# Performance work log

Measured on AMD Instinct MI355X. Metric: run time of the kernel, lower is better.

The kernel has to match this reference:

```python
import jax, jax.numpy as jnp
import numpy as np

B, S, D, O, R, E = 2, 4096, 4096, 4096, 256, 8
SCALE = 2.0

def setup_inputs() -> dict:
    key = jax.random.key(0)
    k_x, k_t, k_w, k_a, k_b = jax.random.split(key, 5)
    x = jax.random.normal(k_x, (B, S, D), dtype=jnp.float32)
    token_type = jax.random.randint(k_t, (S,), 0, E, dtype=jnp.int64)
    # weight_base: [out_features, in_features] as required by F.linear
    weight_base = jax.random.normal(k_w, (O, D), dtype=jnp.float32) * 0.02
    # LoRA stacks: lora_A [E, D, R], lora_B [E, R, O]. (Original inits B to zeros;
    # we use small random values so the LoRA path is numerically non-trivial.)
    lora_A = jax.random.normal(k_a, (E, D, R), dtype=jnp.float32) * 0.02
    lora_B = jax.random.normal(k_b, (E, R, O), dtype=jnp.float32) * 0.02
    return {"x": x, "weight_base": weight_base, "lora_A": lora_A,
            "lora_B": lora_B, "token_type": token_type}

def reference(x, weight_base, lora_A, lora_B, token_type):
    # base GEMM: F.linear(x, W) = x @ W.T  -> [B, S, O]
    base = jnp.einsum('bsd,od->bso', x, weight_base)
    # per-expert low-rank projection: h[e,b,s,:] = x[b,s,:] @ lora_A[e]
    h = jnp.einsum('bsd,edr->ebsr', x, lora_A)              # [E, B, S, R]
    # dispatch: zero out tokens not routed to expert e (token_type partitions S)
    onehot = jax.nn.one_hot(token_type, E, dtype=x.dtype)   # [S, E]
    h = h * onehot.T[:, None, :, None]                      # mask over (e, s)
    # combine: sum over experts of masked h @ lora_B[e]
    lora = jnp.einsum('ebsr,ero->bso', h, lora_B)           # [B, S, O]
    # every token has token_type in [0, E), so scatter covers all positions:
    # result = base + scale * expert_lora everywhere
    return base + SCALE * lora
```

## Files before the change

### kernel.cpp

```cpp
#include <hip/hip_runtime.h>

#define S_TOK 4096
#define D_DIM 4096
#define O_DIM 4096
#define R_DIM 256
#define E_EXP 8
#define NTOK  8192
#define KSPLIT 4

typedef __bf16 bf16x8 __attribute__((ext_vector_type(8)));
typedef float  f32x4  __attribute__((ext_vector_type(4)));

__device__ __forceinline__ unsigned short f2bf(float f) {
  unsigned int u = __float_as_uint(f);
  u += 0x7FFFu + ((u >> 16) & 1u);
  return (unsigned short)(u >> 16);
}
__device__ __forceinline__ float bf2f(unsigned short h) {
  return __uint_as_float(((unsigned int)h) << 16);
}

__device__ __forceinline__ void gload_lds16(const unsigned short* g, unsigned short* l) {
  __builtin_amdgcn_global_load_lds((const __attribute__((address_space(1))) void*)g,
                                   (__attribute__((address_space(3))) void*)l, 16, 0, 0);
}

#define PIPE_FENCE(N)                                                        \
  do {                                                                       \
    asm volatile("s_waitcnt vmcnt(" #N ")\n\ts_barrier" ::: "memory");       \
    __builtin_amdgcn_sched_barrier(0);                                       \
  } while (0)

__global__ void prologue(const float* __restrict__ x, const float* __restrict__ wb,
                         const float* __restrict__ la, const float* __restrict__ lb,
                         unsigned short* __restrict__ X16, unsigned short* __restrict__ W16,
                         unsigned short* __restrict__ A16t, unsigned short* __restrict__ B16t,
                         const int* __restrict__ tt, int* __restrict__ token_perm,
                         int* __restrict__ inv_perm, int* __restrict__ tile_e,
                         int* __restrict__ tile_j0, int* __restrict__ tile_jend,
                         int* __restrict__ ntiles_out) {
  __shared__ int sm[10256];
  const int b = blockIdx.x, t = threadIdx.x;
  if (b >= 40960) {
    int* ltt   = sm;
    int* lc    = sm + 4096;
    int* ssl   = sm + 6144;
    int* basee = sm + 10240;
    int* cnte  = sm + 10248;
    for (int s = t; s < S_TOK; s += 256) ltt[s] = tt[s];
    __syncthreads();
    int c[8] = {0,0,0,0,0,0,0,0};
    #pragma unroll
    for (int i = 0; i < 16; i++) { int e = ltt[t * 16 + i]; c[e]++; }
    #pragma unroll
    for (int e = 0; e < 8; e++) lc[t * 8 + e] = c[e];
    __syncthreads();
    if (t < 8) {
      int run = 0;
      for (int qq = 0; qq < 256; qq++) { int tmp = lc[qq * 8 + t]; lc[qq * 8 + t] = run; run += tmp; }
      cnte[t] = run;
    }
    __syncthreads();
    if (t == 0) { int tot = 0; for (int e = 0; e < 8; e++) { basee[e] = tot; tot += cnte[e]; } }
    __syncthreads();
    int off[8];
    #pragma unroll
    for (int e = 0; e < 8; e++) off[e] = basee[e] + lc[t * 8 + e];
    #pragma unroll
    for (int i = 0; i < 16; i++) { int s = t * 16 + i; int e = ltt[s]; ssl[off[e]++] = s; }
    __syncthreads();
    for (int j = t; j < NTOK; j += 256) {
      int row = ((j & 1) << 12) + ssl[j >> 1];
      token_perm[j] = row;
      inv_perm[row] = j;
    }
    if (t == 0) {
      int nt = 0;
      for (int e = 0; e < 8; e++) {
        int js = 2 * basee[e], je = js + 2 * cnte[e];
        for (int j0 = js; j0 < je; j0 += 128) {
          tile_e[nt] = e; tile_j0[nt] = j0;
          tile_jend[nt] = (je < j0 + 128) ? je : (j0 + 128);
          nt++;
        }
      }
      *ntiles_out = nt;
    }
    return;
  }
  if (b < 24576) {
    const float* in  = (b < 16384) ? x : wb;
    unsigned short* out = (b < 16384) ? X16 : W16;
    size_t g = (size_t)((b < 16384) ? b : (b - 16384)) * 256 + t;
    const float4* i4 = (const float4*)in;
    float4 a = i4[g * 2], c = i4[g * 2 + 1];
    union { unsigned short h[8]; int4 v; } u;
    u.h[0] = f2bf(a.x); u.h[1] = f2bf(a.y); u.h[2] = f2bf(a.z); u.h[3] = f2bf(a.w);
    u.h[4] = f2bf(c.x); u.h[5] = f2bf(c.y); u.h[6] = f2bf(c.z); u.h[7] = f2bf(c.w);
    ((int4*)out)[g] = u.v;
    return;
  }
  unsigned short (*tile)[33] = (unsigned short (*)[33])sm;
  const float* in; unsigned short* out; int P, Q, pt, qt, e;
  if (b < 32768) {
    int b2 = b - 24576; e = b2 >> 10; int rem = b2 & 1023;
    in = la; out = A16t; P = D_DIM; Q = R_DIM;
    pt = (rem >> 3) * 32; qt = (rem & 7) * 32;
  } else {
    int b3 = b - 32768; e = b3 >> 10; int rem = b3 & 1023;
    in = lb; out = B16t; P = R_DIM; Q = D_DIM;
    pt = (rem & 7) * 32; qt = (rem >> 3) * 32;
  }
  const float* ie = in + (size_t)e * P * Q;
  unsigned short* oe = out + (size_t)e * P * Q;
  int tx = t & 31, ty = t >> 5;
  #pragma unroll
  for (int i = 0; i < 32; i += 8) {
    int p = pt + ty + i, q = qt + tx;
    tile[ty + i][tx] = f2bf(ie[(size_t)p * Q + q]);
  }
  __syncthreads();
  #pragma unroll
  for (int i = 0; i < 32; i += 8) {
    int q = qt + ty + i, p = pt + tx;
    oe[(size_t)q * P + p] = tile[tx][ty + i];
  }
}

template<int FUSED>
__global__ __launch_bounds__(512, 2) void gemm256_dense(
    const unsigned short* __restrict__ A, const unsigned short* __restrict__ B,
    float* __restrict__ C, const unsigned short* __restrict__ lout,
    const int* __restrict__ invp) {
  __shared__ __align__(16) unsigned short ldsA[2][2][8192];
  __shared__ __align__(16) unsigned short ldsB[2][2][8192];
  int b = blockIdx.x;
  int xc = b & 7, q = b >> 3;
  const int bm = (xc >> 1) * 8 + (q >> 3);
  const int bn = (xc & 1) * 8 + (q & 7);
  const int tid = threadIdx.x, l = tid & 63, w = tid >> 6;
  const int wm = w >> 2, wn = w & 3;

  const unsigned short *srcA0, *srcA1, *srcB0, *srcB1;
  {
    int i0 = tid, r0 = i0 >> 2;
    int c0 = ((i0 & 3) * 16) ^ (((r0 >> 1) & 3) << 4);
    srcA0 = A + (size_t)(bm * 256 + r0) * 4096 + (c0 >> 1);
    srcB0 = B + (size_t)(bn * 256 + r0) * 4096 + (c0 >> 1);
    int i1 = 512 + tid, r1 = i1 >> 2;
    int c1 = ((i1 & 3) * 16) ^ (((r1 >> 1) & 3) << 4);
    srcA1 = A + (size_t)(bm * 256 + r1) * 4096 + (c1 >> 1);
    srcB1 = B + (size_t)(bn * 256 + r1) * 4096 + (c1 >> 1);
  }
  const int d0 = tid * 8;

  const int lane15 = l & 15, kb16 = (l >> 4) * 16;
  int offA[8], offB[4];
  #pragma unroll
  for (int m = 0; m < 8; m++) {
    int r = wm * 128 + m * 16 + lane15;
    offA[m] = r * 64 + (kb16 ^ (((r >> 1) & 3) << 4));
  }
  #pragma unroll
  for (int n = 0; n < 4; n++) {
    int r = wn * 64 + n * 16 + lane15;
    offB[n] = r * 64 + (kb16 ^ (((r >> 1) & 3) << 4));
  }

  f32x4 acc[8][4];
  #pragma unroll
  for (int m = 0; m < 8; m++)
    #pragma unroll
    for (int n = 0; n < 4; n++) acc[m][n] = (f32x4){0.f, 0.f, 0.f, 0.f};

  bf16x8 Ab0[4], Ab1[4], Bb0[4], Bb1[4];

#define STAGE_A(tt, kh) do { int _o = (tt) * 64 + (kh) * 32;                  \
    gload_lds16(srcA0 + _o, &ldsA[(tt) & 1][kh][d0]);                         \
    gload_lds16(srcA1 + _o, &ldsA[(tt) & 1][kh][d0 + 4096]); } while (0)
#define STAGE_B(tt, kh) do { int _o = (tt) * 64 + (kh) * 32;                  \
    gload_lds16(srcB0 + _o, &ldsB[(tt) & 1][kh][d0]);                         \
    gload_lds16(srcB1 + _o, &ldsB[(tt) & 1][kh][d0 + 4096]); } while (0)
#define RD_A(RING, QQ, KS, BUF) do {                                          \
    const char* _s = (const char*)&ldsA[RING][KS][0];                         \
    BUF[0] = *(const bf16x8*)(_s + offA[(QQ) * 4 + 0]);                       \
    BUF[1] = *(const bf16x8*)(_s + offA[(QQ) * 4 + 1]);                       \
    BUF[2] = *(const bf16x8*)(_s + offA[(QQ) * 4 + 2]);                       \
    BUF[3] = *(const bf16x8*)(_s + offA[(QQ) * 4 + 3]); } while (0)
#define RD_B(RING, KS, BUF) do {                                              \
    const char* _s = (const char*)&ldsB[RING][KS][0];                         \
    BUF[0] = *(const bf16x8*)(_s + offB[0]);                                  \
    BUF[1] = *(const bf16x8*)(_s + offB[1]);                                  \
    BUF[2] = *(const bf16x8*)(_s + offB[2]);                                  \
    BUF[3] = *(const bf16x8*)(_s + offB[3]); } while (0)
#define PRIO_MFMA(Q, AB, BB) do {                                             \
    __builtin_amdgcn_s_setprio(1);                                            \
    _Pragma("unroll")                                                         \
    for (int mm = 0; mm < 4; mm++)                                            \
      _Pragma("unroll")                                                       \
      for (int nn = 0; nn < 4; nn++)                                          \
        acc[(Q) * 4 + mm][nn] = __builtin_amdgcn_mfma_f32_16x16x32_bf16(      \
            AB[mm], BB[nn], acc[(Q) * 4 + mm][nn], 0, 0, 0);                  \
    __builtin_amdgcn_s_setprio(0); } while (0)

  STAGE_A(0, 0); STAGE_B(0, 0); STAGE_A(0, 1); STAGE_B(0, 1);
  STAGE_A(1, 0); STAGE_B(1, 0);
  PIPE_FENCE(4);
  RD_B(0, 0, Bb0); RD_A(0, 0, 0, Ab0);

  #pragma unroll 1
  for (int t = 0; t < 62; ++t) {
    const int r = t & 1, nr = r ^ 1;
    RD_A(r, 1, 0, Ab1); STAGE_A(t + 1, 1);
    PRIO_MFMA(0, Ab0, Bb0);
    RD_B(r, 1, Bb1); RD_A(r, 0, 1, Ab0); STAGE_B(t + 1, 1);
    PRIO_MFMA(1, Ab1, Bb0);
    PIPE_FENCE(4);
    RD_A(r, 1, 1, Ab1); STAGE_A(t + 2, 0);
    PRIO_MFMA(0, Ab0, Bb1);
    RD_B(nr, 0, Bb0); RD_A(nr, 0, 0, Ab0); STAGE_B(t + 2, 0);
    PRIO_MFMA(1, Ab1, Bb1);
    PIPE_FENCE(4);
  }
  RD_A(0, 1, 0, Ab1); STAGE_A(63, 1); PRIO_MFMA(0, Ab0, Bb0);
  RD_B(0, 1, Bb1); RD_A(0, 0, 1, Ab0); STAGE_B(63, 1); PRIO_MFMA(1, Ab1, Bb0);
  PIPE_FENCE(4);
  RD_A(0, 1, 1, Ab1); PRIO_MFMA(0, Ab0, Bb1);
  RD_B(1, 0, Bb0); RD_A(1, 0, 0, Ab0); PRIO_MFMA(1, Ab1, Bb1);
  PIPE_FENCE(0);
  RD_A(1, 1, 0, Ab1); PRIO_MFMA(0, Ab0, Bb0);
  RD_B(1, 1, Bb1); RD_A(1, 0, 1, Ab0); PRIO_MFMA(1, Ab1, Bb0);
  RD_A(1, 1, 1, Ab1); PRIO_MFMA(0, Ab0, Bb1);
  PRIO_MFMA(1, Ab1, Bb1);

#undef STAGE_A
#undef STAGE_B
#undef RD_A
#undef RD_B
#undef PRIO_MFMA

  const int rowbase = bm * 256 + wm * 128;
  const int colbase = bn * 256 + wn * 64;
  #pragma unroll
  for (int m = 0; m < 8; m++)
    #pragma unroll
    for (int v = 0; v < 4; v++) {
      int rrow = rowbase + m * 16 + (l >> 4) * 4 + v;
      float lv0 = 0.f, lv1 = 0.f, lv2 = 0.f, lv3 = 0.f;
      if (FUSED) {
        int jr = invp[rrow];
        const unsigned short* lr = lout + (size_t)jr * O_DIM + colbase + lane15;
        lv0 = bf2f(lr[0]); lv1 = bf2f(lr[16]); lv2 = bf2f(lr[32]); lv3 = bf2f(lr[48]);
      }
      size_t base = (size_t)rrow * O_DIM + colbase + lane15;
      C[base]      = acc[m][0][v] + lv0;
      C[base + 16] = acc[m][1][v] + lv1;
      C[base + 32] = acc[m][2][v] + lv2;
      C[base + 48] = acc[m][3][v] + lv3;
    }
}

template<int MODE>
__global__ __launch_bounds__(256, 2) void gemm_nt(
    const unsigned short* __restrict__ Aop, const unsigned short* __restrict__ Bop,
    unsigned short* __restrict__ outU,
    const int* __restrict__ perm, const int* __restrict__ tile_e,
    const int* __restrict__ tile_j0, const int* __restrict__ tile_jend,
    const int* __restrict__ ntiles, int K) {
  int bm = blockIdx.x, bn = blockIdx.y;
  if (bm >= *ntiles) return;
  int e = tile_e[bm], j0 = tile_j0[bm], jend = tile_jend[bm];
  const int kc = (MODE == 1) ? blockIdx.z : 0;
  const int t = threadIdx.x, l = t & 63, w = t >> 6;
  const int wm = w >> 1, wn = w & 1;
  __shared__ __align__(16) unsigned short ldsA[4][4096];
  __shared__ __align__(16) unsigned short ldsB[4][4096];

  const unsigned short *sA0, *sA1, *sB0, *sB1;
  {
    int i0 = t, r0 = i0 >> 2;
    int c0 = ((i0 & 3) * 16) ^ (((r0 >> 1) & 3) << 4);
    int i1 = 256 + t, r1 = i1 >> 2;
    int c1 = ((i1 & 3) * 16) ^ (((r1 >> 1) & 3) << 4);
    int ja = j0 + r0; if (ja > jend - 1) ja = jend - 1;
    int jb = j0 + r1; if (jb > jend - 1) jb = jend - 1;
    int g0 = (MODE == 1) ? perm[ja] : ja;
    int g1 = (MODE == 1) ? perm[jb] : jb;
    sA0 = Aop + (size_t)g0 * K + kc * 1024 + (c0 >> 1);
    sA1 = Aop + (size_t)g1 * K + kc * 1024 + (c1 >> 1);
    const unsigned short* bp = Bop + ((MODE == 1) ? (size_t)e * R_DIM * D_DIM
                                                  : (size_t)e * O_DIM * R_DIM);
    sB0 = bp + (size_t)(bn * 128 + r0) * K + kc * 1024 + (c0 >> 1);
    sB1 = bp + (size_t)(bn * 128 + r1) * K + kc * 1024 + (c1 >> 1);
  }
  const int d0 = t * 8;

  const int lane15 = l & 15, kb16 = (l >> 4) * 16;
  int offA[4], offB[4];
  #pragma unroll
  for (int m = 0; m < 4; m++) {
    int r = wm * 64 + m * 16 + lane15;
    offA[m] = r * 64 + (kb16 ^ (((r >> 1) & 3) << 4));
  }
  #pragma unroll
  for (int n = 0; n < 4; n++) {
    int r = wn * 64 + n * 16 + lane15;
    offB[n] = r * 64 + (kb16 ^ (((r >> 1) & 3) << 4));
  }

  f32x4 acc[4][4];
  #pragma unroll
  for (int m = 0; m < 4; m++)
    #pragma unroll
    for (int n = 0; n < 4; n++) acc[m][n] = (f32x4){0.f, 0.f, 0.f, 0.f};

  auto stage = [&](int tt) {
    const int ring = tt & 3;
    const int go = tt * 32;
    gload_lds16(sA0 + go, &ldsA[ring][d0]);
    gload_lds16(sA1 + go, &ldsA[ring][d0 + 2048]);
    gload_lds16(sB0 + go, &ldsB[ring][d0]);
    gload_lds16(sB1 + go, &ldsB[ring][d0 + 2048]);
  };

  auto body = [&](int ring) {
    const char* bA = (const char*)&ldsA[ring][0];
    const char* bB = (const char*)&ldsB[ring][0];
    bf16x8 a[4], bb[4];
    #pragma unroll
    for (int m = 0; m < 4; m++) a[m] = *(const bf16x8*)(bA + offA[m]);
    #pragma unroll
    for (int n = 0; n < 4; n++) bb[n] = *(const bf16x8*)(bB + offB[n]);
    __builtin_amdgcn_s_setprio(1);
    #pragma unroll
    for (int m = 0; m < 4; m++)
      #pragma unroll
      for (int n = 0; n < 4; n++)
        acc[m][n] = __builtin_amdgcn_mfma_f32_16x16x32_bf16(a[m], bb[n], acc[m][n], 0, 0, 0);
    __builtin_amdgcn_s_setprio(0);
  };

  const int nk = (MODE == 1) ? 32 : (K / 32);
  stage(0); stage(1); stage(2);
  PIPE_FENCE(8);
  #pragma unroll 1
  for (int kt = 0; kt < nk - 3; ++kt) {
    stage(kt + 3);
    body(kt & 3);
    PIPE_FENCE(8);
  }
  body((nk - 3) & 3);
  PIPE_FENCE(4);
  body((nk - 2) & 3);
  PIPE_FENCE(0);
  body((nk - 1) & 3);

  const int rowbase = j0 + wm * 64;
  const int colbase = bn * 128 + wn * 64;
  #pragma unroll
  for (int m = 0; m < 4; m++) {
    #pragma unroll
    for (int n = 0; n < 4; n++) {
      #pragma unroll
      for (int v = 0; v < 4; v++) {
        int r = rowbase + m * 16 + (l >> 4) * 4 + v;
        int cc = colbase + n * 16 + lane15;
        if (r < jend) {
          if (MODE == 1) {
            outU[(size_t)kc * (NTOK * R_DIM) + (size_t)r * R_DIM + cc] = f2bf(acc[m][n][v]);
          } else {
            outU[(size_t)r * O_DIM + cc] = f2bf(2.0f * acc[m][n][v]);
          }
        }
      }
    }
  }
}

__global__ void reduce_h(const unsigned short* __restrict__ hp, unsigned short* __restrict__ h16) {
  size_t g = (size_t)blockIdx.x * 256 + threadIdx.x;
  float s[8] = {0,0,0,0,0,0,0,0};
  #pragma unroll
  for (int c = 0; c < KSPLIT; c++) {
    int4 v = ((const int4*)hp)[g + (size_t)c * (NTOK * R_DIM / 8)];
    const unsigned short* us = (const unsigned short*)&v;
    #pragma unroll
    for (int i = 0; i < 8; i++) s[i] += bf2f(us[i]);
  }
  union { unsigned short h[8]; int4 v; } u;
  #pragma unroll
  for (int i = 0; i < 8; i++) u.h[i] = f2bf(s[i]);
  ((int4*)h16)[g] = u.v;
}

#define X16_OFF   ((size_t)0)
#define W16_OFF   ((size_t)67108864)
#define A16T_OFF  ((size_t)100663296)
#define B16T_OFF  ((size_t)117440512)
#define H16S_OFF  ((size_t)134217728)
#define PERM_OFF  ((size_t)138412032)
#define INVP_OFF  ((size_t)138444800)
#define TILEE_OFF ((size_t)138477568)
#define TILEJ0_OFF ((size_t)138478080)
#define TILEJE_OFF ((size_t)138478592)
#define NT_OFF    ((size_t)138479104)
#define HP16_OFF  ((size_t)138479616)
#define LOUT_OFF  ((size_t)155256832)

extern "C" void kernel_launch(void* const* d_in, const int* in_sizes, int n_in,
                              void* d_out, int out_size, void* d_ws, size_t ws_size,
                              hipStream_t stream) {
  const float* x  = (const float*)d_in[0];
  const float* wb = (const float*)d_in[1];
  const float* la = (const float*)d_in[2];
  const float* lb = (const float*)d_in[3];
  const int* tok  = (const int*)d_in[4];
  float* out = (float*)d_out;

  char* ws = (char*)d_ws;
  unsigned short* X16  = (unsigned short*)(ws + X16_OFF);
  unsigned short* W16  = (unsigned short*)(ws + W16_OFF);
  unsigned short* A16t = (unsigned short*)(ws + A16T_OFF);
  unsigned short* B16t = (unsigned short*)(ws + B16T_OFF);
  unsigned short* H16s = (unsigned short*)(ws + H16S_OFF);
  unsigned short* HP16 = (unsigned short*)(ws + HP16_OFF);
  unsigned short* LOUT = (unsigned short*)(ws + LOUT_OFF);
  int* perm  = (int*)(ws + PERM_OFF);
  int* invp  = (int*)(ws + INVP_OFF);
  int* tl_e  = (int*)(ws + TILEE_OFF);
  int* tl_j0 = (int*)(ws + TILEJ0_OFF);
  int* tl_je = (int*)(ws + TILEJE_OFF);
  int* nt    = (int*)(ws + NT_OFF);

  prologue<<<40961, 256, 0, stream>>>(x, wb, la, lb, X16, W16, A16t, B16t,
                                      tok, perm, invp, tl_e, tl_j0, tl_je, nt);

  gemm_nt<1><<<dim3(71, 2, KSPLIT), 256, 0, stream>>>(X16, A16t, HP16,
                                                      perm, tl_e, tl_j0, tl_je, nt, D_DIM);
  reduce_h<<<1024, 256, 0, stream>>>(HP16, H16s);
  gemm_nt<3><<<dim3(71, 32), 256, 0, stream>>>(H16s, B16t, LOUT,
                                               perm, tl_e, tl_j0, tl_je, nt, R_DIM);
  gemm256_dense<1><<<512, 512, 0, stream>>>(X16, W16, out, LOUT, invp);
}
```

Baseline: 458.7 us.

## Restructure dense GEMM main loop into four quadrant phases with new LDS layout

The base dense GEMM now stages each LDS buffer by output quadrant (64-row A halves and 32-row B halves, full 64-wide K per row) instead of by K-half. Each of the four phases per K-tile reads its A/B fragments, issues one quadrant's global-to-LDS load, barriers, then runs 16 MFMAs on that quadrant. The XOR swizzle changes to a row-based 8-way pattern to avoid LDS bank conflicts. The aim is finer-grained interleaving of loads and MFMAs. The cost is extra s_barrier instructions per tile and different vmcnt fence depths.

```diff
diff --git a/kernel.cpp b/kernel.cpp
--- a/kernel.cpp
+++ b/kernel.cpp
@@ -28,6 +28,11 @@
 #define PIPE_FENCE(N)                                                        \
   do {                                                                       \
     asm volatile("s_waitcnt vmcnt(" #N ")\n\ts_barrier" ::: "memory");       \
+    __builtin_amdgcn_sched_barrier(0);                                       \
+  } while (0)
+#define BARX                                                                 \
+  do {                                                                       \
+    asm volatile("s_barrier" ::: "memory");                                  \
     __builtin_amdgcn_sched_barrier(0);                                       \
   } while (0)
 
@@ -128,7 +133,7 @@
 }
 
 template<int FUSED>
-__global__ __launch_bounds__(512, 2) void gemm256_dense(
+__global__ __launch_bounds__(512, 2) void gemm256_q(
     const unsigned short* __restrict__ A, const unsigned short* __restrict__ B,
     float* __restrict__ C, const unsigned short* __restrict__ lout,
     const int* __restrict__ invp) {
@@ -141,30 +146,27 @@
   const int tid = threadIdx.x, l = tid & 63, w = tid >> 6;
   const int wm = w >> 2, wn = w & 3;
 
-  const unsigned short *srcA0, *srcA1, *srcB0, *srcB1;
-  {
-    int i0 = tid, r0 = i0 >> 2;
-    int c0 = ((i0 & 3) * 16) ^ (((r0 >> 1) & 3) << 4);
-    srcA0 = A + (size_t)(bm * 256 + r0) * 4096 + (c0 >> 1);
-    srcB0 = B + (size_t)(bn * 256 + r0) * 4096 + (c0 >> 1);
-    int i1 = 512 + tid, r1 = i1 >> 2;
-    int c1 = ((i1 & 3) * 16) ^ (((r1 >> 1) & 3) << 4);
-    srcA1 = A + (size_t)(bm * 256 + r1) * 4096 + (c1 >> 1);
-    srcB1 = B + (size_t)(bn * 256 + r1) * 4096 + (c1 >> 1);
-  }
-  const int d0 = tid * 8;
-
-  const int lane15 = l & 15, kb16 = (l >> 4) * 16;
-  int offA[8], offB[4];
-  #pragma unroll
-  for (int m = 0; m < 8; m++) {
-    int r = wm * 128 + m * 16 + lane15;
-    offA[m] = r * 64 + (kb16 ^ (((r >> 1) & 3) << 4));
-  }
-  #pragma unroll
-  for (int n = 0; n < 4; n++) {
-    int r = wn * 64 + n * 16 + lane15;
-    offB[n] = r * 64 + (kb16 ^ (((r >> 1) & 3) << 4));
+  const int u0 = tid >> 3, j0s = tid & 7;
+  const int ksw = ((j0s ^ (u0 & 7)) * 8);
+  const unsigned short* srcA0 = A + (size_t)(bm * 256 + u0) * 4096 + ksw;
+  const unsigned short* srcA1 = A + (size_t)(bm * 256 + 128 + u0) * 4096 + ksw;
+  const int brB0 = ((u0 >> 5) << 6) + (u0 & 31);
+  const int brB1 = (((64 + u0) >> 5) << 6) + (u0 & 31);
+  const unsigned short* srcB0 = B + (size_t)(bn * 256 + brB0) * 4096 + ksw;
+  const unsigned short* srcB1 = B + (size_t)(bn * 256 + brB1) * 4096 + ksw;
+
+  const int lane15 = l & 15, kbase = (l >> 4) * 16;
+  const int lsw = (lane15 & 7) << 4;
+  int offA[4], offB[2];
+  #pragma unroll
+  for (int j = 0; j < 4; j++) {
+    int u = wm * 64 + j * 16 + lane15;
+    offA[j] = u * 128 + (kbase ^ lsw);
+  }
+  #pragma unroll
+  for (int i = 0; i < 2; i++) {
+    int u = wn * 32 + i * 16 + lane15;
+    offB[i] = u * 128 + (kbase ^ lsw);
   }
 
   f32x4 acc[8][4];
@@ -173,71 +175,74 @@
     #pragma unroll
     for (int n = 0; n < 4; n++) acc[m][n] = (f32x4){0.f, 0.f, 0.f, 0.f};
 
-  bf16x8 Ab0[4], Ab1[4], Bb0[4], Bb1[4];
-
-#define STAGE_A(tt, kh) do { int _o = (tt) * 64 + (kh) * 32;                  \
-    gload_lds16(srcA0 + _o, &ldsA[(tt) & 1][kh][d0]);                         \
-    gload_lds16(srcA1 + _o, &ldsA[(tt) & 1][kh][d0 + 4096]); } while (0)
-#define STAGE_B(tt, kh) do { int _o = (tt) * 64 + (kh) * 32;                  \
-    gload_lds16(srcB0 + _o, &ldsB[(tt) & 1][kh][d0]);                         \
-    gload_lds16(srcB1 + _o, &ldsB[(tt) & 1][kh][d0 + 4096]); } while (0)
-#define RD_A(RING, QQ, KS, BUF) do {                                          \
-    const char* _s = (const char*)&ldsA[RING][KS][0];                         \
-    BUF[0] = *(const bf16x8*)(_s + offA[(QQ) * 4 + 0]);                       \
-    BUF[1] = *(const bf16x8*)(_s + offA[(QQ) * 4 + 1]);                       \
-    BUF[2] = *(const bf16x8*)(_s + offA[(QQ) * 4 + 2]);                       \
-    BUF[3] = *(const bf16x8*)(_s + offA[(QQ) * 4 + 3]); } while (0)
-#define RD_B(RING, KS, BUF) do {                                              \
-    const char* _s = (const char*)&ldsB[RING][KS][0];                         \
-    BUF[0] = *(const bf16x8*)(_s + offB[0]);                                  \
-    BUF[1] = *(const bf16x8*)(_s + offB[1]);                                  \
-    BUF[2] = *(const bf16x8*)(_s + offB[2]);                                  \
-    BUF[3] = *(const bf16x8*)(_s + offB[3]); } while (0)
-#define PRIO_MFMA(Q, AB, BB) do {                                             \
+#define STAGE_A(TT, H) do {                                                   \
+    gload_lds16(srcA0 + (size_t)(H) * 262144 + (TT) * 64,                     \
+                &ldsA[(TT) & 1][H][tid * 8]);                                 \
+    gload_lds16(srcA1 + (size_t)(H) * 262144 + (TT) * 64,                     \
+                &ldsA[(TT) & 1][H][4096 + tid * 8]); } while (0)
+#define STAGE_B(TT, H) do {                                                   \
+    gload_lds16(srcB0 + (size_t)(H) * 131072 + (TT) * 64,                     \
+                &ldsB[(TT) & 1][H][tid * 8]);                                 \
+    gload_lds16(srcB1 + (size_t)(H) * 131072 + (TT) * 64,                     \
+                &ldsB[(TT) & 1][H][4096 + tid * 8]); } while (0)
+#define NOSTAGE do {} while (0)
+
+#define PH(RING, QM, QN, STAGE_STMT, TRAILER) do {                            \
+    const char* _a = (const char*)&ldsA[RING][QM][0];                         \
+    const char* _b = (const char*)&ldsB[RING][QN][0];                         \
+    bf16x8 a0_[4], a1_[4], b0_[2], b1_[2];                                    \
+    _Pragma("unroll")                                                         \
+    for (int j = 0; j < 4; j++) {                                             \
+      a0_[j] = *(const bf16x8*)(_a + offA[j]);                                \
+      a1_[j] = *(const bf16x8*)(_a + (offA[j] ^ 64));                         \
+    }                                                                         \
+    _Pragma("unroll")                                                         \
+    for (int i = 0; i < 2; i++) {                                             \
+      b0_[i] = *(const bf16x8*)(_b + offB[i]);                                \
+      b1_[i] = *(const bf16x8*)(_b + (offB[i] ^ 64));                         \
+    }                                                                         \
+    STAGE_STMT;                                                               \
+    asm volatile("s_barrier\n\ts_waitcnt lgkmcnt(0)" ::: "memory");           \
+    __builtin_amdgcn_sched_barrier(0);                                        \
     __builtin_amdgcn_s_setprio(1);                                            \
     _Pragma("unroll")                                                         \
-    for (int mm = 0; mm < 4; mm++)                                            \
+    for (int j = 0; j < 4; j++)                                               \
       _Pragma("unroll")                                                       \
-      for (int nn = 0; nn < 4; nn++)                                          \
-        acc[(Q) * 4 + mm][nn] = __builtin_amdgcn_mfma_f32_16x16x32_bf16(      \
-            AB[mm], BB[nn], acc[(Q) * 4 + mm][nn], 0, 0, 0);                  \
-    __builtin_amdgcn_s_setprio(0); } while (0)
+      for (int i = 0; i < 2; i++) {                                           \
+        acc[(QM) * 4 + j][(QN) * 2 + i] = __builtin_amdgcn_mfma_f32_16x16x32_bf16( \
+            a0_[j], b0_[i], acc[(QM) * 4 + j][(QN) * 2 + i], 0, 0, 0);        \
+        acc[(QM) * 4 + j][(QN) * 2 + i] = __builtin_amdgcn_mfma_f32_16x16x32_bf16( \
+            a1_[j], b1_[i], acc[(QM) * 4 + j][(QN) * 2 + i], 0, 0, 0);        \
+      }                                                                       \
+    __builtin_amdgcn_s_setprio(0);                                            \
+    TRAILER;                                                                  \
+  } while (0)
 
   STAGE_A(0, 0); STAGE_B(0, 0); STAGE_A(0, 1); STAGE_B(0, 1);
   STAGE_A(1, 0); STAGE_B(1, 0);
-  PIPE_FENCE(4);
-  RD_B(0, 0, Bb0); RD_A(0, 0, 0, Ab0);
+  PIPE_FENCE(8);
 
   #pragma unroll 1
   for (int t = 0; t < 62; ++t) {
-    const int r = t & 1, nr = r ^ 1;
-    RD_A(r, 1, 0, Ab1); STAGE_A(t + 1, 1);
-    PRIO_MFMA(0, Ab0, Bb0);
-    RD_B(r, 1, Bb1); RD_A(r, 0, 1, Ab0); STAGE_B(t + 1, 1);
-    PRIO_MFMA(1, Ab1, Bb0);
-    PIPE_FENCE(4);
-    RD_A(r, 1, 1, Ab1); STAGE_A(t + 2, 0);
-    PRIO_MFMA(0, Ab0, Bb1);
-    RD_B(nr, 0, Bb0); RD_A(nr, 0, 0, Ab0); STAGE_B(t + 2, 0);
-    PRIO_MFMA(1, Ab1, Bb1);
-    PIPE_FENCE(4);
-  }
-  RD_A(0, 1, 0, Ab1); STAGE_A(63, 1); PRIO_MFMA(0, Ab0, Bb0);
-  RD_B(0, 1, Bb1); RD_A(0, 0, 1, Ab0); STAGE_B(63, 1); PRIO_MFMA(1, Ab1, Bb0);
-  PIPE_FENCE(4);
-  RD_A(0, 1, 1, Ab1); PRIO_MFMA(0, Ab0, Bb1);
-  RD_B(1, 0, Bb0); RD_A(1, 0, 0, Ab0); PRIO_MFMA(1, Ab1, Bb1);
-  PIPE_FENCE(0);
-  RD_A(1, 1, 0, Ab1); PRIO_MFMA(0, Ab0, Bb0);
-  RD_B(1, 1, Bb1); RD_A(1, 0, 1, Ab0); PRIO_MFMA(1, Ab1, Bb0);
-  RD_A(1, 1, 1, Ab1); PRIO_MFMA(0, Ab0, Bb1);
-  PRIO_MFMA(1, Ab1, Bb1);
+    const int r = t & 1;
+    PH(r, 0, 0, STAGE_A(t + 1, 1), PIPE_FENCE(6));
+    PH(r, 0, 1, STAGE_B(t + 1, 1), BARX);
+    PH(r, 1, 0, STAGE_A(t + 2, 0), BARX);
+    PH(r, 1, 1, STAGE_B(t + 2, 0), PIPE_FENCE(8));
+  }
+  PH(0, 0, 0, STAGE_A(63, 1), PIPE_FENCE(6));
+  PH(0, 0, 1, STAGE_B(63, 1), BARX);
+  PH(0, 1, 0, NOSTAGE, BARX);
+  PH(0, 1, 1, NOSTAGE, PIPE_FENCE(4));
+  PH(1, 0, 0, NOSTAGE, PIPE_FENCE(0));
+  PH(1, 0, 1, NOSTAGE, BARX);
+  PH(1, 1, 0, NOSTAGE, BARX);
+  PH(1, 1, 1, NOSTAGE, NOSTAGE);
 
 #undef STAGE_A
 #undef STAGE_B
-#undef RD_A
-#undef RD_B
-#undef PRIO_MFMA
+#undef NOSTAGE
+#undef PH
 
   const int rowbase = bm * 256 + wm * 128;
   const int colbase = bn * 256 + wn * 64;
@@ -440,5 +445,5 @@
   reduce_h<<<1024, 256, 0, stream>>>(HP16, H16s);
   gemm_nt<3><<<dim3(71, 32), 256, 0, stream>>>(H16s, B16t, LOUT,
                                                perm, tl_e, tl_j0, tl_je, nt, R_DIM);
-  gemm256_dense<1><<<512, 512, 0, stream>>>(X16, W16, out, LOUT, invp);
-}
+  gemm256_q<1><<<512, 512, 0, stream>>>(X16, W16, out, LOUT, invp);
+}
```

After: 528.1 us. +15.1%, slower.

## Fuse LoRA-B expansion into base GEMM over expert-sorted token rows

Applied to the files above, without the earlier changes.

The separate LoRA-B grouped GEMM, which wrote a bf16 intermediate that the dense GEMM then read back through an inverse permutation, is removed. The dense GEMM now processes rows in expert-sorted order. After the base K loop, each tile runs an extra K=256 pass per expert segment it overlaps, with masked rows reading from a zero buffer, and results are scattered back through perm. This drops one kernel launch and a full [8192x4096] intermediate write and read. In exchange it adds a gathered A-operand load, a non-pipelined extra loop with full fences, and extra MFMA work for tiles that span several experts.

```diff
diff --git a/kernel.cpp b/kernel.cpp
--- a/kernel.cpp
+++ b/kernel.cpp
@@ -30,15 +30,22 @@
     asm volatile("s_waitcnt vmcnt(" #N ")\n\ts_barrier" ::: "memory");       \
     __builtin_amdgcn_sched_barrier(0);                                       \
   } while (0)
+#define BARX                                                                 \
+  do {                                                                       \
+    asm volatile("s_barrier" ::: "memory");                                  \
+    __builtin_amdgcn_sched_barrier(0);                                       \
+  } while (0)
 
 __global__ void prologue(const float* __restrict__ x, const float* __restrict__ wb,
                          const float* __restrict__ la, const float* __restrict__ lb,
                          unsigned short* __restrict__ X16, unsigned short* __restrict__ W16,
                          unsigned short* __restrict__ A16t, unsigned short* __restrict__ B16t,
                          const int* __restrict__ tt, int* __restrict__ token_perm,
-                         int* __restrict__ inv_perm, int* __restrict__ tile_e,
-                         int* __restrict__ tile_j0, int* __restrict__ tile_jend,
-                         int* __restrict__ ntiles_out) {
+                         int* __restrict__ tile_e, int* __restrict__ tile_j0,
+                         int* __restrict__ tile_jend, int* __restrict__ ntiles_out,
+                         int* __restrict__ seg_n, int* __restrict__ seg_e,
+                         int* __restrict__ seg_lo, int* __restrict__ seg_hi,
+                         unsigned short* __restrict__ zp) {
   __shared__ int sm[10256];
   const int b = blockIdx.x, t = threadIdx.x;
   if (b >= 40960) {
@@ -47,6 +54,7 @@
     int* ssl   = sm + 6144;
     int* basee = sm + 10240;
     int* cnte  = sm + 10248;
+    if (t < 64) ((long long*)zp)[t] = 0;
     for (int s = t; s < S_TOK; s += 256) ltt[s] = tt[s];
     __syncthreads();
     int c[8] = {0,0,0,0,0,0,0,0};
@@ -70,9 +78,7 @@
     for (int i = 0; i < 16; i++) { int s = t * 16 + i; int e = ltt[s]; ssl[off[e]++] = s; }
     __syncthreads();
     for (int j = t; j < NTOK; j += 256) {
-      int row = ((j & 1) << 12) + ssl[j >> 1];
-      token_perm[j] = row;
-      inv_perm[row] = j;
+      token_perm[j] = ((j & 1) << 12) + ssl[j >> 1];
     }
     if (t == 0) {
       int nt = 0;
@@ -85,6 +91,17 @@
         }
       }
       *ntiles_out = nt;
+      for (int p = 0; p < 32; p++) {
+        int plo = p * 256, phi = plo + 256, ns = 0;
+        for (int e = 0; e < 8; e++) {
+          int es = 2 * basee[e], ee = es + 2 * cnte[e];
+          int lo = es > plo ? es : plo;
+          int hi = ee < phi ? ee : phi;
+          if (lo < hi) { seg_e[p * 8 + ns] = e; seg_lo[p * 8 + ns] = lo - plo;
+                         seg_hi[p * 8 + ns] = hi - plo; ns++; }
+        }
+        seg_n[p] = ns;
+      }
     }
     return;
   }
@@ -127,11 +144,13 @@
   }
 }
 
-template<int FUSED>
-__global__ __launch_bounds__(512, 2) void gemm256_dense(
+__global__ __launch_bounds__(512, 2) void gemm256_s(
     const unsigned short* __restrict__ A, const unsigned short* __restrict__ B,
-    float* __restrict__ C, const unsigned short* __restrict__ lout,
-    const int* __restrict__ invp) {
+    const unsigned short* __restrict__ H, const unsigned short* __restrict__ Bl,
+    float* __restrict__ C, const int* __restrict__ perm,
+    const int* __restrict__ seg_n, const int* __restrict__ seg_e,
+    const int* __restrict__ seg_lo, const int* __restrict__ seg_hi,
+    const unsigned short* __restrict__ zp) {
   __shared__ __align__(16) unsigned short ldsA[2][2][8192];
   __shared__ __align__(16) unsigned short ldsB[2][2][8192];
   int b = blockIdx.x;
@@ -141,18 +160,16 @@
   const int tid = threadIdx.x, l = tid & 63, w = tid >> 6;
   const int wm = w >> 2, wn = w & 3;
 
-  const unsigned short *srcA0, *srcA1, *srcB0, *srcB1;
-  {
-    int i0 = tid, r0 = i0 >> 2;
-    int c0 = ((i0 & 3) * 16) ^ (((r0 >> 1) & 3) << 4);
-    srcA0 = A + (size_t)(bm * 256 + r0) * 4096 + (c0 >> 1);
-    srcB0 = B + (size_t)(bn * 256 + r0) * 4096 + (c0 >> 1);
-    int i1 = 512 + tid, r1 = i1 >> 2;
-    int c1 = ((i1 & 3) * 16) ^ (((r1 >> 1) & 3) << 4);
-    srcA1 = A + (size_t)(bm * 256 + r1) * 4096 + (c1 >> 1);
-    srcB1 = B + (size_t)(bn * 256 + r1) * 4096 + (c1 >> 1);
-  }
-  const int d0 = tid * 8;
+  const int i0 = tid, r0 = i0 >> 2;
+  const int c0 = ((i0 & 3) * 16) ^ (((r0 >> 1) & 3) << 4);
+  const int i1 = 512 + tid, r1 = i1 >> 2;
+  const int c1 = ((i1 & 3) * 16) ^ (((r1 >> 1) & 3) << 4);
+  const int sr0 = perm[bm * 256 + r0];
+  const int sr1 = perm[bm * 256 + r1];
+  const unsigned short* srcA0 = A + (size_t)sr0 * 4096 + (c0 >> 1);
+  const unsigned short* srcA1 = A + (size_t)sr1 * 4096 + (c1 >> 1);
+  const unsigned short* srcB0 = B + (size_t)(bn * 256 + r0) * 4096 + (c0 >> 1);
+  const unsigned short* srcB1 = B + (size_t)(bn * 256 + r1) * 4096 + (c1 >> 1);
 
   const int lane15 = l & 15, kb16 = (l >> 4) * 16;
   int offA[8], offB[4];
@@ -176,11 +193,11 @@
   bf16x8 Ab0[4], Ab1[4], Bb0[4], Bb1[4];
 
 #define STAGE_A(tt, kh) do { int _o = (tt) * 64 + (kh) * 32;                  \
-    gload_lds16(srcA0 + _o, &ldsA[(tt) & 1][kh][d0]);                         \
-    gload_lds16(srcA1 + _o, &ldsA[(tt) & 1][kh][d0 + 4096]); } while (0)
+    gload_lds16(srcA0 + _o, &ldsA[(tt) & 1][kh][tid * 8]);                    \
+    gload_lds16(srcA1 + _o, &ldsA[(tt) & 1][kh][tid * 8 + 4096]); } while (0)
 #define STAGE_B(tt, kh) do { int _o = (tt) * 64 + (kh) * 32;                  \
-    gload_lds16(srcB0 + _o, &ldsB[(tt) & 1][kh][d0]);                         \
-    gload_lds16(srcB1 + _o, &ldsB[(tt) & 1][kh][d0 + 4096]); } while (0)
+    gload_lds16(srcB0 + _o, &ldsB[(tt) & 1][kh][tid * 8]);                    \
+    gload_lds16(srcB1 + _o, &ldsB[(tt) & 1][kh][tid * 8 + 4096]); } while (0)
 #define RD_A(RING, QQ, KS, BUF) do {                                          \
     const char* _s = (const char*)&ldsA[RING][KS][0];                         \
     BUF[0] = *(const bf16x8*)(_s + offA[(QQ) * 4 + 0]);                       \
@@ -233,6 +250,39 @@
   RD_A(1, 1, 1, Ab1); PRIO_MFMA(0, Ab0, Bb1);
   PRIO_MFMA(1, Ab1, Bb1);
 
+  const int pn = seg_n[bm];
+  #pragma unroll 1
+  for (int s = 0; s < pn; ++s) {
+    const int eE = seg_e[bm * 8 + s], lo = seg_lo[bm * 8 + s], hi = seg_hi[bm * 8 + s];
+    const unsigned short* h0 = (r0 >= lo && r0 < hi)
+        ? H + (size_t)(bm * 256 + r0) * 256 + (c0 >> 1) : zp + (c0 >> 1);
+    const unsigned short* h1 = (r1 >= lo && r1 < hi)
+        ? H + (size_t)(bm * 256 + r1) * 256 + (c1 >> 1) : zp + (c1 >> 1);
+    const unsigned short* be0 = Bl + (size_t)eE * (O_DIM * R_DIM)
+        + (size_t)(bn * 256 + r0) * 256 + (c0 >> 1);
+    const unsigned short* be1 = Bl + (size_t)eE * (O_DIM * R_DIM)
+        + (size_t)(bn * 256 + r1) * 256 + (c1 >> 1);
+    #pragma unroll 1
+    for (int kt = 0; kt < 4; ++kt) {
+      const int rg = kt & 1;
+      const int o0 = kt * 64, o1 = kt * 64 + 32;
+      gload_lds16(h0 + o0,  &ldsA[rg][0][tid * 8]);
+      gload_lds16(h1 + o0,  &ldsA[rg][0][tid * 8 + 4096]);
+      gload_lds16(h0 + o1,  &ldsA[rg][1][tid * 8]);
+      gload_lds16(h1 + o1,  &ldsA[rg][1][tid * 8 + 4096]);
+      gload_lds16(be0 + o0, &ldsB[rg][0][tid * 8]);
+      gload_lds16(be1 + o0, &ldsB[rg][0][tid * 8 + 4096]);
+      gload_lds16(be0 + o1, &ldsB[rg][1][tid * 8]);
+      gload_lds16(be1 + o1, &ldsB[rg][1][tid * 8 + 4096]);
+      PIPE_FENCE(0);
+      RD_B(rg, 0, Bb0); RD_A(rg, 0, 0, Ab0); PRIO_MFMA(0, Ab0, Bb0);
+      RD_A(rg, 1, 0, Ab1);                   PRIO_MFMA(1, Ab1, Bb0);
+      RD_B(rg, 1, Bb1); RD_A(rg, 0, 1, Ab0); PRIO_MFMA(0, Ab0, Bb1);
+      RD_A(rg, 1, 1, Ab1);                   PRIO_MFMA(1, Ab1, Bb1);
+      BARX;
+    }
+  }
+
 #undef STAGE_A
 #undef STAGE_B
 #undef RD_A
@@ -246,31 +296,26 @@
     #pragma unroll
     for (int v = 0; v < 4; v++) {
       int rrow = rowbase + m * 16 + (l >> 4) * 4 + v;
-      float lv0 = 0.f, lv1 = 0.f, lv2 = 0.f, lv3 = 0.f;
-      if (FUSED) {
-        int jr = invp[rrow];
-        const unsigned short* lr = lout + (size_t)jr * O_DIM + colbase + lane15;
-        lv0 = bf2f(lr[0]); lv1 = bf2f(lr[16]); lv2 = bf2f(lr[32]); lv3 = bf2f(lr[48]);
-      }
-      size_t base = (size_t)rrow * O_DIM + colbase + lane15;
-      C[base]      = acc[m][0][v] + lv0;
-      C[base + 16] = acc[m][1][v] + lv1;
-      C[base + 32] = acc[m][2][v] + lv2;
-      C[base + 48] = acc[m][3][v] + lv3;
-    }
-}
-
-template<int MODE>
-__global__ __launch_bounds__(256, 2) void gemm_nt(
+      int orow = perm[rrow];
+      size_t base = (size_t)orow * O_DIM + colbase + lane15;
+      C[base]      = acc[m][0][v];
+      C[base + 16] = acc[m][1][v];
+      C[base + 32] = acc[m][2][v];
+      C[base + 48] = acc[m][3][v];
+    }
+}
+
+__global__ __launch_bounds__(256, 2) void gemm_nt1(
     const unsigned short* __restrict__ Aop, const unsigned short* __restrict__ Bop,
     unsigned short* __restrict__ outU,
     const int* __restrict__ perm, const int* __restrict__ tile_e,
     const int* __restrict__ tile_j0, const int* __restrict__ tile_jend,
-    const int* __restrict__ ntiles, int K) {
+    const int* __restrict__ ntiles) {
+  const int K = D_DIM;
   int bm = blockIdx.x, bn = blockIdx.y;
   if (bm >= *ntiles) return;
   int e = tile_e[bm], j0 = tile_j0[bm], jend = tile_jend[bm];
-  const int kc = (MODE == 1) ? blockIdx.z : 0;
+  const int kc = blockIdx.z;
   const int t = threadIdx.x, l = t & 63, w = t >> 6;
   const int wm = w >> 1, wn = w & 1;
   __shared__ __align__(16) unsigned short ldsA[4][4096];
@@ -284,12 +329,10 @@
     int c1 = ((i1 & 3) * 16) ^ (((r1 >> 1) & 3) << 4);
     int ja = j0 + r0; if (ja > jend - 1) ja = jend - 1;
     int jb = j0 + r1; if (jb > jend - 1) jb = jend - 1;
-    int g0 = (MODE == 1) ? perm[ja] : ja;
-    int g1 = (MODE == 1) ? perm[jb] : jb;
+    int g0 = perm[ja], g1 = perm[jb];
     sA0 = Aop + (size_t)g0 * K + kc * 1024 + (c0 >> 1);
     sA1 = Aop + (size_t)g1 * K + kc * 1024 + (c1 >> 1);
-    const unsigned short* bp = Bop + ((MODE == 1) ? (size_t)e * R_DIM * D_DIM
-                                                  : (size_t)e * O_DIM * R_DIM);
+    const unsigned short* bp = Bop + (size_t)e * R_DIM * D_DIM;
     sB0 = bp + (size_t)(bn * 128 + r0) * K + kc * 1024 + (c0 >> 1);
     sB1 = bp + (size_t)(bn * 128 + r1) * K + kc * 1024 + (c1 >> 1);
   }
@@ -340,7 +383,7 @@
     __builtin_amdgcn_s_setprio(0);
   };
 
-  const int nk = (MODE == 1) ? 32 : (K / 32);
+  const int nk = 32;
   stage(0); stage(1); stage(2);
   PIPE_FENCE(8);
   #pragma unroll 1
@@ -365,13 +408,8 @@
       for (int v = 0; v < 4; v++) {
         int r = rowbase + m * 16 + (l >> 4) * 4 + v;
         int cc = colbase + n * 16 + lane15;
-        if (r < jend) {
-          if (MODE == 1) {
-            outU[(size_t)kc * (NTOK * R_DIM) + (size_t)r * R_DIM + cc] = f2bf(acc[m][n][v]);
-          } else {
-            outU[(size_t)r * O_DIM + cc] = f2bf(2.0f * acc[m][n][v]);
-          }
-        }
+        if (r < jend)
+          outU[(size_t)kc * (NTOK * R_DIM) + (size_t)r * R_DIM + cc] = f2bf(acc[m][n][v]);
       }
     }
   }
@@ -389,7 +427,7 @@
   }
   union { unsigned short h[8]; int4 v; } u;
   #pragma unroll
-  for (int i = 0; i < 8; i++) u.h[i] = f2bf(s[i]);
+  for (int i = 0; i < 8; i++) u.h[i] = f2bf(2.0f * s[i]);
   ((int4*)h16)[g] = u.v;
 }
 
@@ -399,13 +437,16 @@
 #define B16T_OFF  ((size_t)117440512)
 #define H16S_OFF  ((size_t)134217728)
 #define PERM_OFF  ((size_t)138412032)
-#define INVP_OFF  ((size_t)138444800)
 #define TILEE_OFF ((size_t)138477568)
 #define TILEJ0_OFF ((size_t)138478080)
 #define TILEJE_OFF ((size_t)138478592)
 #define NT_OFF    ((size_t)138479104)
 #define HP16_OFF  ((size_t)138479616)
-#define LOUT_OFF  ((size_t)155256832)
+#define SEGN_OFF  ((size_t)155256832)
+#define SEGE_OFF  ((size_t)155257344)
+#define SEGLO_OFF ((size_t)155258368)
+#define SEGHI_OFF ((size_t)155259392)
+#define ZERO_OFF  ((size_t)155260416)
 
 extern "C" void kernel_launch(void* const* d_in, const int* in_sizes, int n_in,
                               void* d_out, int out_size, void* d_ws, size_t ws_size,
@@ -424,21 +465,25 @@
   unsigned short* B16t = (unsigned short*)(ws + B16T_OFF);
   unsigned short* H16s = (unsigned short*)(ws + H16S_OFF);
   unsigned short* HP16 = (unsigned short*)(ws + HP16_OFF);
-  unsigned short* LOUT = (unsigned short*)(ws + LOUT_OFF);
+  unsigned short* ZP   = (unsigned short*)(ws + ZERO_OFF);
   int* perm  = (int*)(ws + PERM_OFF);
-  int* invp  = (int*)(ws + INVP_OFF);
   int* tl_e  = (int*)(ws + TILEE_OFF);
   int* tl_j0 = (int*)(ws + TILEJ0_OFF);
   int* tl_je = (int*)(ws + TILEJE_OFF);
   int* nt    = (int*)(ws + NT_OFF);
+  int* sgn   = (int*)(ws + SEGN_OFF);
+  int* sge   = (int*)(ws + SEGE_OFF);
+  int* sglo  = (int*)(ws + SEGLO_OFF);
+  int* sghi  = (int*)(ws + SEGHI_OFF);
 
   prologue<<<40961, 256, 0, stream>>>(x, wb, la, lb, X16, W16, A16t, B16t,
-                                      tok, perm, invp, tl_e, tl_j0, tl_je, nt);
-
-  gemm_nt<1><<<dim3(71, 2, KSPLIT), 256, 0, stream>>>(X16, A16t, HP16,
-                                                      perm, tl_e, tl_j0, tl_je, nt, D_DIM);
+                                      tok, perm, tl_e, tl_j0, tl_je, nt,
+                                      sgn, sge, sglo, sghi, ZP);
+
+  gemm_nt1<<<dim3(71, 2, KSPLIT), 256, 0, stream>>>(X16, A16t, HP16,
+                                                    perm, tl_e, tl_j0, tl_je, nt);
   reduce_h<<<1024, 256, 0, stream>>>(HP16, H16s);
-  gemm_nt<3><<<dim3(71, 32), 256, 0, stream>>>(H16s, B16t, LOUT,
-                                               perm, tl_e, tl_j0, tl_je, nt, R_DIM);
-  gemm256_dense<1><<<512, 512, 0, stream>>>(X16, W16, out, LOUT, invp);
-}
+
+  gemm256_s<<<512, 512, 0, stream>>>(X16, W16, H16s, B16t, out, perm,
+                                     sgn, sge, sglo, sghi, ZP);
+}
```

Measured after the change: 405.3 us, median of 2. -11.7%, faster.
